# Performance work log

Measured on AMD Instinct MI355X. Metric: run time of the kernel, lower is better.

Reference implementation:

```python
import jax, jax.numpy as jnp
import numpy as np
import math

B, N, E, D = 8, 2048, 2048, 128
MAX_K = 8
HYPER_DIM = 128
LN_EPS = 1e-5


def _sinusoidal_pe(max_pos, dim):
    pe = np.zeros((max_pos, dim), dtype=np.float32)
    position = np.arange(max_pos, dtype=np.float32)[:, None]
    div_term = np.exp(np.arange(0, dim, 2, dtype=np.float32) * (-math.log(10000.0) / dim))
    pe[:, 0::2] = np.sin(position * div_term)
    pe[:, 1::2] = np.cos(position * div_term)
    return jnp.asarray(pe)


def setup_inputs() -> dict:
    key = jax.random.key(0)
    ks = jax.random.split(key, 24)
    s = 0.05
    inp = {
        'x_v': jax.random.normal(ks[0], (B, N, D), jnp.float32),
        'x_e': jax.random.normal(ks[1], (B, E, D), jnp.float32),
        'incidence': (jax.random.uniform(ks[2], (B, N, E), jnp.float32) < 0.01).astype(jnp.float32),
        'suffix_normalizer': jax.random.uniform(ks[3], (B, N), jnp.float32) * 20.0,
        'edge_orders': 1 + jax.random.randint(ks[4], (B, E), 0, MAX_K),
        'node_mask': jax.random.randint(ks[5], (B, N), 0, 2) > 0,
        'edge_mask': jax.random.randint(ks[6], (B, E), 0, 2) > 0,
        'pe1_table': _sinusoidal_pe(MAX_K + 1, D),
        'pe2_table': _sinusoidal_pe(2, D),
        'bias_b': jax.random.uniform(ks[7], (1, D), jnp.float32, -1, 1) / math.sqrt(D),
    }
    i = 8
    for m in ('mlp1', 'mlp2', 'mlp3'):
        inp[m + '_W1'] = jax.random.normal(ks[i], (D, HYPER_DIM), jnp.float32) * s; i += 1
        inp[m + '_b1'] = jnp.zeros((HYPER_DIM,), jnp.float32)
        inp[m + '_W2'] = jax.random.normal(ks[i], (HYPER_DIM, D), jnp.float32) * s; i += 1
        inp[m + '_b2'] = jnp.zeros((D,), jnp.float32)
    for n in ('norm1', 'norm2', 'norm3'):
        inp[n + '_g'] = jnp.ones((D,), jnp.float32)
        inp[n + '_b'] = jnp.zeros((D,), jnp.float32)
    return inp


def _ln(x, g, b):
    mu = jnp.mean(x, axis=-1, keepdims=True)
    var = jnp.mean(jnp.square(x - mu), axis=-1, keepdims=True)
    return (x - mu) * jax.lax.rsqrt(var + LN_EPS) * g + b


def _mlp(x, W1, b1, W2, b2):
    return jax.nn.relu(x @ W1 + b1) @ W2 + b2


def reference(x_v, x_e, incidence, suffix_normalizer, edge_orders, node_mask, edge_mask,
              pe1_table, pe2_table, bias_b,
              mlp1_W1, mlp1_b1, mlp1_W2, mlp1_b2,
              mlp2_W1, mlp2_b1, mlp2_W2, mlp2_b2,
              mlp3_W1, mlp3_b1, mlp3_W2, mlp3_b2,
              norm1_g, norm1_b, norm2_g, norm2_b, norm3_g, norm3_b):
    nm = node_mask[..., None]  # [B,N,1]
    em = edge_mask[..., None]  # [B,E,1]
    x_v = jnp.where(nm, x_v, 0.0)
    x_e = jnp.where(em, x_e, 0.0)
    pe1_k1 = pe1_table[1][None, None, :]          # [1,1,D]
    pe1_k = pe1_table[edge_orders]                # [B,E,D]
    x_v = x_v + _mlp(_ln(x_v, norm1_g, norm1_b) + pe1_k1, mlp1_W1, mlp1_b1, mlp1_W2, mlp1_b2)
    x_e = x_e + _mlp(_ln(x_e, norm1_g, norm1_b) + pe1_k, mlp1_W1, mlp1_b1, mlp1_W2, mlp1_b2)
    x_v = jnp.where(nm, x_v, 0.0)
    x_e = jnp.where(em, x_e, 0.0)
    agg = jnp.einsum('bne,bed->bnd', incidence, x_e)
    x1 = x_v + agg / (1.0 + suffix_normalizer[..., None])
    pe2_s1 = pe2_table[1][None, None, :]
    x1 = x1 + _mlp(_ln(x1, norm2_g, norm2_b) + pe2_s1, mlp2_W1, mlp2_b1, mlp2_W2, mlp2_b2)
    x = jnp.where(nm, x1, 0.0)
    x = x + _mlp(_ln(x, norm3_g, norm3_b), mlp3_W1, mlp3_b1, mlp3_W2, mlp3_b2)
    x = x + bias_b
    x = jnp.where(nm, x, 0.0)
    return x
```

## Files before the change

### kernel.cpp

```cpp
#include <hip/hip_runtime.h>
#include <stdint.h>

#define BB 8
#define NN 2048
#define EE 2048
#define DD 128
#define ROWS 32
#define RBP 132
#define NTHREADS 256
#define WMAT_U32 8192
#define SCANB 2048
#define LCAP 64

typedef __attribute__((ext_vector_type(8))) short bf16x8;
typedef __attribute__((ext_vector_type(4))) float f32x4;

__device__ inline unsigned bf16rne(float f) {
    unsigned u = __float_as_uint(f);
    return (u + 0x7fffu + ((u >> 16) & 1u)) >> 16;
}
__device__ inline float bf16lo(unsigned u) { return __uint_as_float(u << 16); }
__device__ inline float bf16hi(unsigned u) { return __uint_as_float(u & 0xffff0000u); }

#define SWZ(b) ((b) ^ ((((b) >> 8) & 7) << 4))

struct __align__(16) Smem {
    float rowbuf[ROWS][RBP];
    unsigned h[ROWS * DD / 2];
    unsigned scw[4][64];
    int rmask[ROWS];
    int ords[ROWS];
};

__device__ inline void block_load_rows(Smem& s, const float* __restrict__ src,
                                       const int* __restrict__ mask) {
    int t = threadIdx.x;
    for (int idx = t; idx < ROWS * 32; idx += NTHREADS) {
        int r = idx >> 5, c4 = (idx & 31) * 4;
        float4 v = make_float4(0.f, 0.f, 0.f, 0.f);
        if (mask[r] != 0) v = *(const float4*)&src[r * DD + c4];
        *(float4*)&s.rowbuf[r][c4] = v;
    }
    __syncthreads();
}

__device__ inline void block_ln(Smem& s, const float* __restrict__ gw,
                                const float* __restrict__ bw,
                                const float* __restrict__ pe_base, bool per_row_pe) {
    int t = threadIdx.x;
    int gr = t >> 3, g = t & 7;
    int base = g * 16;
    float x[16];
    float4* xp = (float4*)x;
    xp[0] = *(const float4*)&s.rowbuf[gr][base + 0];
    xp[1] = *(const float4*)&s.rowbuf[gr][base + 4];
    xp[2] = *(const float4*)&s.rowbuf[gr][base + 8];
    xp[3] = *(const float4*)&s.rowbuf[gr][base + 12];
    float s1 = 0.f, s2 = 0.f;
    #pragma unroll
    for (int i = 0; i < 16; i++) { s1 += x[i]; s2 += x[i] * x[i]; }
    #pragma unroll
    for (int off = 1; off < 8; off <<= 1) {
        s1 += __shfl_xor(s1, off, 64);
        s2 += __shfl_xor(s2, off, 64);
    }
    float mu = s1 * (1.f / 128.f);
    float var = s2 * (1.f / 128.f) - mu * mu;
    float rstd = rsqrtf(var + 1e-5f);
    const float* pe = nullptr;
    if (pe_base) pe = per_row_pe ? (pe_base + (size_t)s.ords[gr] * DD) : pe_base;
    unsigned p[8];
    #pragma unroll
    for (int j = 0; j < 8; j++) {
        int k0 = base + 2 * j;
        float v0 = (x[2 * j] - mu) * rstd * gw[k0] + bw[k0];
        float v1 = (x[2 * j + 1] - mu) * rstd * gw[k0 + 1] + bw[k0 + 1];
        if (pe) { v0 += pe[k0]; v1 += pe[k0 + 1]; }
        p[j] = bf16rne(v0) | (bf16rne(v1) << 16);
    }
    char* hb = (char*)s.h;
    int byte0 = gr * 256 + g * 32;
    uint4 lo = make_uint4(p[0], p[1], p[2], p[3]);
    uint4 hi = make_uint4(p[4], p[5], p[6], p[7]);
    *(uint4*)(hb + SWZ(byte0)) = lo;
    *(uint4*)(hb + SWZ(byte0 + 16)) = hi;
    __syncthreads();
}

template <bool TO_H>
__device__ inline void block_mm_core(Smem& s, const bf16x8 bfr[2][4],
                                     const float* __restrict__ bias) {
    int t = threadIdx.x;
    int w = t >> 6, l = t & 63;
    int lm = l & 15, lk = l >> 4;
    const char* hb = (const char*)s.h;
    bf16x8 afr[2][4];
    #pragma unroll
    for (int mb = 0; mb < 2; mb++) {
        int row = mb * 16 + lm;
        #pragma unroll
        for (int kb = 0; kb < 4; kb++) {
            afr[mb][kb] = *(const bf16x8*)(hb + SWZ(row * 256 + kb * 64 + lk * 16));
        }
    }
    f32x4 acc[2][2];
    #pragma unroll
    for (int mb = 0; mb < 2; mb++)
        #pragma unroll
        for (int nbl = 0; nbl < 2; nbl++)
            acc[mb][nbl] = (f32x4){0.f, 0.f, 0.f, 0.f};
    #pragma unroll
    for (int kb = 0; kb < 4; kb++)
        #pragma unroll
        for (int mb = 0; mb < 2; mb++)
            #pragma unroll
            for (int nbl = 0; nbl < 2; nbl++)
                acc[mb][nbl] = __builtin_amdgcn_mfma_f32_16x16x32_bf16(
                    afr[mb][kb], bfr[nbl][kb], acc[mb][nbl], 0, 0, 0);
    float bcol0 = bias[w * 32 + lm];
    float bcol1 = bias[w * 32 + 16 + lm];
    __syncthreads();
    if (TO_H) {
        char* hw = (char*)s.h;
        #pragma unroll
        for (int mb = 0; mb < 2; mb++)
            #pragma unroll
            for (int nbl = 0; nbl < 2; nbl++) {
                int col = w * 32 + nbl * 16 + lm;
                float bc = nbl ? bcol1 : bcol0;
                #pragma unroll
                for (int j = 0; j < 4; j++) {
                    int row = mb * 16 + lk * 4 + j;
                    float v = fmaxf(acc[mb][nbl][j] + bc, 0.f);
                    *(unsigned short*)(hw + SWZ(row * 256 + col * 2)) =
                        (unsigned short)bf16rne(v);
                }
            }
    } else {
        #pragma unroll
        for (int mb = 0; mb < 2; mb++)
            #pragma unroll
            for (int nbl = 0; nbl < 2; nbl++) {
                int col = w * 32 + nbl * 16 + lm;
                float bc = nbl ? bcol1 : bcol0;
                #pragma unroll
                for (int j = 0; j < 4; j++) {
                    int row = mb * 16 + lk * 4 + j;
                    s.rowbuf[row][col] += acc[mb][nbl][j] + bc;
                }
            }
    }
    __syncthreads();
}

template <bool TO_H>
__device__ inline void block_mm(Smem& s, const unsigned* __restrict__ WT,
                                const float* __restrict__ bias) {
    int t = threadIdx.x;
    int w = t >> 6, l = t & 63;
    int lm = l & 15, lk = l >> 4;
    bf16x8 bfr[2][4];
    const uint4* wt4 = (const uint4*)WT;
    #pragma unroll
    for (int nbl = 0; nbl < 2; nbl++) {
        int n = w * 32 + nbl * 16 + lm;
        #pragma unroll
        for (int kb = 0; kb < 4; kb++) {
            uint4 u = wt4[n * 16 + kb * 4 + lk];
            bfr[nbl][kb] = *(bf16x8*)&u;
        }
    }
    block_mm_core<TO_H>(s, bfr, bias);
}

template <bool TO_H>
__device__ inline void block_mm_f32w(Smem& s, const float* __restrict__ Wf,
                                     const float* __restrict__ bias) {
    int t = threadIdx.x;
    int w = t >> 6, l = t & 63;
    int lm = l & 15, lk = l >> 4;
    bf16x8 bfr[2][4];
    #pragma unroll
    for (int nbl = 0; nbl < 2; nbl++) {
        int n = w * 32 + nbl * 16 + lm;
        #pragma unroll
        for (int kb = 0; kb < 4; kb++) {
            int k0 = kb * 32 + lk * 8;
            unsigned pk[4];
            #pragma unroll
            for (int jp = 0; jp < 4; jp++) {
                float a = Wf[(size_t)(k0 + 2 * jp) * DD + n];
                float b = Wf[(size_t)(k0 + 2 * jp + 1) * DD + n];
                pk[jp] = bf16rne(a) | (bf16rne(b) << 16);
            }
            uint4 u = make_uint4(pk[0], pk[1], pk[2], pk[3]);
            bfr[nbl][kb] = *(bf16x8*)&u;
        }
    }
    block_mm_core<TO_H>(s, bfr, bias);
}

__device__ inline void scan_rows(Smem& s, const float* __restrict__ inc,
                                 const int* __restrict__ nmask,
                                 unsigned* __restrict__ lists, int* __restrict__ cnts,
                                 int wid, int nwaves) {
    int l = threadIdx.x & 63;
    int w = threadIdx.x >> 6;
    unsigned* sc = s.scw[w];
    unsigned long long lmlt = (1ull << l) - 1ull;
    for (int grow = wid; grow < BB * NN; grow += nwaves) {
        if (nmask[grow] == 0) continue;
        const float4* ir = (const float4*)(inc + (size_t)grow * EE);
        float4 v[8];
        #pragma unroll
        for (int i = 0; i < 8; i++) v[i] = ir[l + 64 * i];
        int total = 0;
        #pragma unroll
        for (int i = 0; i < 8; i++) {
            #pragma unroll
            for (int c = 0; c < 4; c++) {
                float val = (c == 0) ? v[i].x : (c == 1) ? v[i].y : (c == 2) ? v[i].z : v[i].w;
                bool nz = (val != 0.f);
                unsigned long long msk = __ballot(nz);
                if (nz) {
                    int pos = total + __popcll(msk & lmlt);
                    if (pos < LCAP) sc[pos] = (unsigned)((l + 64 * i) * 4 + c);
                }
                total += __popcll(msk);
            }
        }
        if (total > LCAP) total = LCAP;
        asm volatile("s_waitcnt lgkmcnt(0)" ::: "memory");
        if (l < 16) {
            uint4 q = *(const uint4*)&sc[4 * l];
            *(uint4*)&lists[(size_t)grow * LCAP + 4 * l] = q;
        }
        if (l == 0) cnts[grow] = total;
    }
}

__device__ inline void block_gather(Smem& s, int rowbase, int bb,
                                    const unsigned* __restrict__ lists,
                                    const int* __restrict__ cnts,
                                    const unsigned* __restrict__ e2pk,
                                    const float* __restrict__ sn) {
    int t = threadIdx.x;
    int w = t >> 6, l = t & 63;
    const unsigned* e2b = e2pk + (size_t)bb * (EE * (DD / 2));
    for (int r = w; r < ROWS; r += 4) {
        if (s.rmask[r] == 0) continue;
        int grow = rowbase + r;
        int cnt = cnts[grow];
        unsigned pk = (l < cnt) ? lists[(size_t)grow * LCAP + l] : 0u;
        float ax = 0.f, ay = 0.f;
        for (int j0 = 0; j0 < cnt; j0 += 8) {
            int nn = cnt - j0;
            unsigned uv[8];
            #pragma unroll
            for (int u = 0; u < 8; u++) {
                unsigned e = __shfl(pk, j0 + u, 64);
                uv[u] = (u < nn) ? e2b[(size_t)e * 64 + l] : 0u;
            }
            #pragma unroll
            for (int u = 0; u < 8; u++) { ax += bf16lo(uv[u]); ay += bf16hi(uv[u]); }
        }
        float inv = 1.f / (1.f + sn[grow]);
        float2* rb = (float2*)&s.rowbuf[r][2 * l];
        float2 cur = *rb;
        cur.x += ax * inv;
        cur.y += ay * inv;
        *rb = cur;
    }
    __syncthreads();
}

__global__ __launch_bounds__(NTHREADS) void k1_kernel(
    const float* __restrict__ x_e, const float* __restrict__ x_v,
    const int* __restrict__ emask, const int* __restrict__ nmask,
    const int* __restrict__ eord, const float* __restrict__ pe1,
    const float* __restrict__ inc,
    const float* __restrict__ n1g, const float* __restrict__ n1b,
    const float* __restrict__ W11, const float* __restrict__ b11,
    const float* __restrict__ W12, const float* __restrict__ b12,
    const float* __restrict__ W21, const float* __restrict__ W22,
    const float* __restrict__ W31, const float* __restrict__ W32,
    unsigned* __restrict__ WT,
    unsigned* __restrict__ e2pk, float* __restrict__ v2out,
    unsigned* __restrict__ lists, int* __restrict__ cnts) {
    __shared__ Smem s;
    int bid = blockIdx.x;
    int t = threadIdx.x;
    if (bid < SCANB) {
        int gtid = bid * NTHREADS + t;
        if (gtid < 4 * WMAT_U32) {
            int mat = gtid >> 13;
            int idx = gtid & (WMAT_U32 - 1);
            int n = idx >> 6, j = idx & 63;
            const float* W = mat == 0 ? W21 : mat == 1 ? W22 : mat == 2 ? W31 : W32;
            float a = W[(2 * j) * DD + n];
            float b = W[(2 * j + 1) * DD + n];
            WT[gtid] = bf16rne(a) | (bf16rne(b) << 16);
        }
        int wid = bid * 4 + (t >> 6);
        scan_rows(s, inc, nmask, lists, cnts, wid, SCANB * 4);
        return;
    }
    int lb = bid - SCANB;
    bool isEdge = lb < (BB * EE / ROWS);
    if (!isEdge) lb -= BB * EE / ROWS;
    int bb = lb & 7;
    int r0 = (lb >> 3) * ROWS;
    int rowbase = bb * EE + r0;
    const int* mask = isEdge ? emask : nmask;
    if (t < ROWS) {
        s.rmask[t] = mask[rowbase + t];
        if (isEdge) {
            int o = eord[rowbase + t];
            s.ords[t] = o < 0 ? 0 : (o > 8 ? 8 : o);
        }
    }
    block_load_rows(s, (isEdge ? x_e : x_v) + (size_t)rowbase * DD, mask + rowbase);
    block_ln(s, n1g, n1b, isEdge ? pe1 : (pe1 + DD), isEdge);
    block_mm_f32w<true>(s, W11, b11);
    block_mm_f32w<false>(s, W12, b12);
    if (isEdge) {
        unsigned* dst = e2pk + (size_t)rowbase * (DD / 2);
        for (int idx = t; idx < ROWS * 16; idx += NTHREADS) {
            int r = idx >> 4, q = idx & 15;
            uint4 o = make_uint4(0u, 0u, 0u, 0u);
            if (s.rmask[r] != 0) {
                const float* rp = &s.rowbuf[r][q * 8];
                o.x = bf16rne(rp[0]) | (bf16rne(rp[1]) << 16);
                o.y = bf16rne(rp[2]) | (bf16rne(rp[3]) << 16);
                o.z = bf16rne(rp[4]) | (bf16rne(rp[5]) << 16);
                o.w = bf16rne(rp[6]) | (bf16rne(rp[7]) << 16);
            }
            *(uint4*)&dst[r * 64 + q * 4] = o;
        }
    } else {
        for (int idx = t; idx < ROWS * 32; idx += NTHREADS) {
            int r = idx >> 5, c4 = (idx & 31) * 4;
            float4 v = make_float4(0.f, 0.f, 0.f, 0.f);
            if (s.rmask[r] != 0) v = *(const float4*)&s.rowbuf[r][c4];
            *(float4*)&v2out[(size_t)(rowbase + r) * DD + c4] = v;
        }
    }
}

__global__ __launch_bounds__(NTHREADS) void k2_kernel(
    const float* __restrict__ v2, const int* __restrict__ nmask,
    const float* __restrict__ sn,
    const float* __restrict__ pe2, const float* __restrict__ biasb,
    const float* __restrict__ n2g, const float* __restrict__ n2b,
    const float* __restrict__ n3g, const float* __restrict__ n3b,
    const unsigned* __restrict__ WT,
    const float* __restrict__ b21, const float* __restrict__ b22,
    const float* __restrict__ b31, const float* __restrict__ b32,
    const unsigned* __restrict__ e2pk, const unsigned* __restrict__ lists,
    const int* __restrict__ cnts, float* __restrict__ out) {
    __shared__ Smem s;
    int bid = blockIdx.x;
    int bb = bid & 7;
    int n0 = (bid >> 3) * ROWS;
    int rowbase = bb * NN + n0;
    int t = threadIdx.x;
    if (t < ROWS) s.rmask[t] = nmask[rowbase + t];
    block_load_rows(s, v2 + (size_t)rowbase * DD, nmask + rowbase);
    block_gather(s, rowbase, bb, lists, cnts, e2pk, sn);
    block_ln(s, n2g, n2b, pe2 + DD, false);
    block_mm<true>(s, WT + 0 * WMAT_U32, b21);
    block_mm<false>(s, WT + 1 * WMAT_U32, b22);
    block_ln(s, n3g, n3b, nullptr, false);
    block_mm<true>(s, WT + 2 * WMAT_U32, b31);
    block_mm<false>(s, WT + 3 * WMAT_U32, b32);
    for (int idx = t; idx < ROWS * 32; idx += NTHREADS) {
        int r = idx >> 5, c4 = (idx & 31) * 4;
        float4 v = make_float4(0.f, 0.f, 0.f, 0.f);
        if (s.rmask[r] != 0) {
            v = *(const float4*)&s.rowbuf[r][c4];
            float4 bbv = *(const float4*)&biasb[c4];
            v.x += bbv.x; v.y += bbv.y; v.z += bbv.z; v.w += bbv.w;
        }
        *(float4*)&out[(size_t)(rowbase + r) * DD + c4] = v;
    }
}

extern "C" void kernel_launch(void* const* d_in, const int* in_sizes, int n_in,
                              void* d_out, int out_size, void* d_ws, size_t ws_size,
                              hipStream_t stream) {
    const float* x_v   = (const float*)d_in[0];
    const float* x_e   = (const float*)d_in[1];
    const float* inc   = (const float*)d_in[2];
    const float* sn    = (const float*)d_in[3];
    const int*   eord  = (const int*)d_in[4];
    const int*   nmask = (const int*)d_in[5];
    const int*   emask = (const int*)d_in[6];
    const float* pe1   = (const float*)d_in[7];
    const float* pe2   = (const float*)d_in[8];
    const float* biasb = (const float*)d_in[9];
    const float* W11   = (const float*)d_in[10];
    const float* b11   = (const float*)d_in[11];
    const float* W12   = (const float*)d_in[12];
    const float* b12   = (const float*)d_in[13];
    const float* W21   = (const float*)d_in[14];
    const float* b21   = (const float*)d_in[15];
    const float* W22   = (const float*)d_in[16];
    const float* b22   = (const float*)d_in[17];
    const float* W31   = (const float*)d_in[18];
    const float* b31   = (const float*)d_in[19];
    const float* W32   = (const float*)d_in[20];
    const float* b32   = (const float*)d_in[21];
    const float* n1g   = (const float*)d_in[22];
    const float* n1b   = (const float*)d_in[23];
    const float* n2g   = (const float*)d_in[24];
    const float* n2b   = (const float*)d_in[25];
    const float* n3g   = (const float*)d_in[26];
    const float* n3b   = (const float*)d_in[27];

    unsigned* e2pk  = (unsigned*)d_ws;
    unsigned* WT    = e2pk + (size_t)BB * EE * (DD / 2);
    unsigned* lists = WT + 4 * WMAT_U32;
    int*      cnts  = (int*)(lists + (size_t)BB * NN * LCAP);
    float*    out   = (float*)d_out;

    dim3 blk(NTHREADS);
    k1_kernel<<<dim3(SCANB + 2 * BB * EE / ROWS), blk, 0, stream>>>(
        x_e, x_v, emask, nmask, eord, pe1, inc,
        n1g, n1b, W11, b11, W12, b12, W21, W22, W31, W32,
        WT, e2pk, out, lists, cnts);
    k2_kernel<<<dim3(BB * NN / ROWS), blk, 0, stream>>>(
        out, nmask, sn, pe2, biasb,
        n2g, n2b, n3g, n3b,
        WT, b21, b22, b31, b32,
        e2pk, lists, cnts, out);
}
```

Before: 65.87 us.

## Replace sparse incidence scan and gather with dense bf16 MFMA aggregation GEMM

```diff
diff --git a/kernel.cpp b/kernel.cpp
--- a/kernel.cpp
+++ b/kernel.cpp
@@ -9,8 +9,6 @@
 #define RBP 132
 #define NTHREADS 256
 #define WMAT_U32 8192
-#define SCANB 2048
-#define LCAP 64
 
 typedef __attribute__((ext_vector_type(8))) short bf16x8;
 typedef __attribute__((ext_vector_type(4))) float f32x4;
@@ -19,21 +17,23 @@
     unsigned u = __float_as_uint(f);
     return (u + 0x7fffu + ((u >> 16) & 1u)) >> 16;
 }
-__device__ inline float bf16lo(unsigned u) { return __uint_as_float(u << 16); }
-__device__ inline float bf16hi(unsigned u) { return __uint_as_float(u & 0xffff0000u); }
 
 #define SWZ(b) ((b) ^ ((((b) >> 8) & 7) << 4))
 
 struct __align__(16) Smem {
     float rowbuf[ROWS][RBP];
     unsigned h[ROWS * DD / 2];
-    unsigned scw[4][64];
+    float ssn[ROWS];
     int rmask[ROWS];
     int ords[ROWS];
 };
 
-__device__ inline void block_load_rows(Smem& s, const float* __restrict__ src,
-                                       const int* __restrict__ mask) {
+__device__ inline unsigned pack01(float a, float b) {
+    return (__float_as_uint(a) >> 16) | (__float_as_uint(b) & 0xffff0000u);
+}
+
+__device__ inline void load_rows32(Smem& s, const float* __restrict__ src,
+                                   const int* __restrict__ mask) {
     int t = threadIdx.x;
     for (int idx = t; idx < ROWS * 32; idx += NTHREADS) {
         int r = idx >> 5, c4 = (idx & 31) * 4;
@@ -44,9 +44,9 @@
     __syncthreads();
 }
 
-__device__ inline void block_ln(Smem& s, const float* __restrict__ gw,
-                                const float* __restrict__ bw,
-                                const float* __restrict__ pe_base, bool per_row_pe) {
+__device__ inline void ln32(Smem& s, const float* __restrict__ gw,
+                            const float* __restrict__ bw,
+                            const float* __restrict__ pe_base, bool per_row_pe) {
     int t = threadIdx.x;
     int gr = t >> 3, g = t & 7;
     int base = g * 16;
@@ -88,8 +88,8 @@
 }
 
 template <bool TO_H>
-__device__ inline void block_mm_core(Smem& s, const bf16x8 bfr[2][4],
-                                     const float* __restrict__ bias) {
+__device__ inline void mm32_core(Smem& s, const bf16x8 bfr[2][4],
+                                 const float* __restrict__ bias) {
     int t = threadIdx.x;
     int w = t >> 6, l = t & 63;
     int lm = l & 15, lk = l >> 4;
@@ -99,9 +99,8 @@
     for (int mb = 0; mb < 2; mb++) {
         int row = mb * 16 + lm;
         #pragma unroll
-        for (int kb = 0; kb < 4; kb++) {
+        for (int kb = 0; kb < 4; kb++)
             afr[mb][kb] = *(const bf16x8*)(hb + SWZ(row * 256 + kb * 64 + lk * 16));
-        }
     }
     f32x4 acc[2][2];
     #pragma unroll
@@ -154,8 +153,8 @@
 }
 
 template <bool TO_H>
-__device__ inline void block_mm(Smem& s, const unsigned* __restrict__ WT,
-                                const float* __restrict__ bias) {
+__device__ inline void mm32(Smem& s, const unsigned* __restrict__ WT,
+                            const float* __restrict__ bias) {
     int t = threadIdx.x;
     int w = t >> 6, l = t & 63;
     int lm = l & 15, lk = l >> 4;
@@ -170,12 +169,12 @@
             bfr[nbl][kb] = *(bf16x8*)&u;
         }
     }
-    block_mm_core<TO_H>(s, bfr, bias);
+    mm32_core<TO_H>(s, bfr, bias);
 }
 
 template <bool TO_H>
-__device__ inline void block_mm_f32w(Smem& s, const float* __restrict__ Wf,
-                                     const float* __restrict__ bias) {
+__device__ inline void mm32_f32w(Smem& s, const float* __restrict__ Wf,
+                                 const float* __restrict__ bias) {
     int t = threadIdx.x;
     int w = t >> 6, l = t & 63;
     int lm = l & 15, lk = l >> 4;
@@ -197,80 +196,63 @@
             bfr[nbl][kb] = *(bf16x8*)&u;
         }
     }
-    block_mm_core<TO_H>(s, bfr, bias);
-}
-
-__device__ inline void scan_rows(Smem& s, const float* __restrict__ inc,
-                                 const int* __restrict__ nmask,
-                                 unsigned* __restrict__ lists, int* __restrict__ cnts,
-                                 int wid, int nwaves) {
-    int l = threadIdx.x & 63;
-    int w = threadIdx.x >> 6;
-    unsigned* sc = s.scw[w];
-    unsigned long long lmlt = (1ull << l) - 1ull;
-    for (int grow = wid; grow < BB * NN; grow += nwaves) {
-        if (nmask[grow] == 0) continue;
-        const float4* ir = (const float4*)(inc + (size_t)grow * EE);
-        float4 v[8];
-        #pragma unroll
-        for (int i = 0; i < 8; i++) v[i] = ir[l + 64 * i];
-        int total = 0;
-        #pragma unroll
-        for (int i = 0; i < 8; i++) {
+    mm32_core<TO_H>(s, bfr, bias);
+}
+
+__device__ inline void agg_gemm(Smem& s, int rowbase, int bb,
+                                const float* __restrict__ inc,
+                                const unsigned* __restrict__ e2T) {
+    int t = threadIdx.x;
+    int w = t >> 6, l = t & 63;
+    int lm = l & 15, lk = l >> 4;
+    const unsigned* eb = e2T + (size_t)bb * (DD * (EE / 2));
+    bool act0 = s.rmask[lm] != 0;
+    bool act1 = s.rmask[16 + lm] != 0;
+    const float* a0p = inc + (size_t)(rowbase + lm) * EE + lk * 8;
+    const float* a1p = inc + (size_t)(rowbase + 16 + lm) * EE + lk * 8;
+    const unsigned* b0p = eb + (size_t)(w * 32 + lm) * (EE / 2) + lk * 4;
+    const unsigned* b1p = eb + (size_t)(w * 32 + 16 + lm) * (EE / 2) + lk * 4;
+    f32x4 acc[2][2];
+    #pragma unroll
+    for (int mb = 0; mb < 2; mb++)
+        #pragma unroll
+        for (int nbl = 0; nbl < 2; nbl++)
+            acc[mb][nbl] = (f32x4){0.f, 0.f, 0.f, 0.f};
+    #pragma unroll 4
+    for (int c = 0; c < 64; c++) {
+        int eo = c * 32;
+        uint4 ua = make_uint4(0u, 0u, 0u, 0u), ub = ua;
+        if (act0) {
+            float4 f0 = *(const float4*)(a0p + eo);
+            float4 f1 = *(const float4*)(a0p + eo + 4);
+            ua = make_uint4(pack01(f0.x, f0.y), pack01(f0.z, f0.w),
+                            pack01(f1.x, f1.y), pack01(f1.z, f1.w));
+        }
+        if (act1) {
+            float4 f0 = *(const float4*)(a1p + eo);
+            float4 f1 = *(const float4*)(a1p + eo + 4);
+            ub = make_uint4(pack01(f0.x, f0.y), pack01(f0.z, f0.w),
+                            pack01(f1.x, f1.y), pack01(f1.z, f1.w));
+        }
+        bf16x8 A0 = *(bf16x8*)&ua;
+        bf16x8 A1 = *(bf16x8*)&ub;
+        bf16x8 B0 = *(const bf16x8*)(b0p + eo / 2);
+        bf16x8 B1 = *(const bf16x8*)(b1p + eo / 2);
+        acc[0][0] = __builtin_amdgcn_mfma_f32_16x16x32_bf16(A0, B0, acc[0][0], 0, 0, 0);
+        acc[0][1] = __builtin_amdgcn_mfma_f32_16x16x32_bf16(A0, B1, acc[0][1], 0, 0, 0);
+        acc[1][0] = __builtin_amdgcn_mfma_f32_16x16x32_bf16(A1, B0, acc[1][0], 0, 0, 0);
+        acc[1][1] = __builtin_amdgcn_mfma_f32_16x16x32_bf16(A1, B1, acc[1][1], 0, 0, 0);
+    }
+    #pragma unroll
+    for (int mb = 0; mb < 2; mb++)
+        #pragma unroll
+        for (int j = 0; j < 4; j++) {
+            int row = mb * 16 + lk * 4 + j;
+            float inv = 1.f / (1.f + s.ssn[row]);
             #pragma unroll
-            for (int c = 0; c < 4; c++) {
-                float val = (c == 0) ? v[i].x : (c == 1) ? v[i].y : (c == 2) ? v[i].z : v[i].w;
-                bool nz = (val != 0.f);
-                unsigned long long msk = __ballot(nz);
-                if (nz) {
-                    int pos = total + __popcll(msk & lmlt);
-                    if (pos < LCAP) sc[pos] = (unsigned)((l + 64 * i) * 4 + c);
-                }
-                total += __popcll(msk);
-            }
-        }
-        if (total > LCAP) total = LCAP;
-        asm volatile("s_waitcnt lgkmcnt(0)" ::: "memory");
-        if (l < 16) {
-            uint4 q = *(const uint4*)&sc[4 * l];
-            *(uint4*)&lists[(size_t)grow * LCAP + 4 * l] = q;
-        }
-        if (l == 0) cnts[grow] = total;
-    }
-}
-
-__device__ inline void block_gather(Smem& s, int rowbase, int bb,
-                                    const unsigned* __restrict__ lists,
-                                    const int* __restrict__ cnts,
-                                    const unsigned* __restrict__ e2pk,
-                                    const float* __restrict__ sn) {
-    int t = threadIdx.x;
-    int w = t >> 6, l = t & 63;
-    const unsigned* e2b = e2pk + (size_t)bb * (EE * (DD / 2));
-    for (int r = w; r < ROWS; r += 4) {
-        if (s.rmask[r] == 0) continue;
-        int grow = rowbase + r;
-        int cnt = cnts[grow];
-        unsigned pk = (l < cnt) ? lists[(size_t)grow * LCAP + l] : 0u;
-        float ax = 0.f, ay = 0.f;
-        for (int j0 = 0; j0 < cnt; j0 += 8) {
-            int nn = cnt - j0;
-            unsigned uv[8];
-            #pragma unroll
-            for (int u = 0; u < 8; u++) {
-                unsigned e = __shfl(pk, j0 + u, 64);
-                uv[u] = (u < nn) ? e2b[(size_t)e * 64 + l] : 0u;
-            }
-            #pragma unroll
-            for (int u = 0; u < 8; u++) { ax += bf16lo(uv[u]); ay += bf16hi(uv[u]); }
-        }
-        float inv = 1.f / (1.f + sn[grow]);
-        float2* rb = (float2*)&s.rowbuf[r][2 * l];
-        float2 cur = *rb;
-        cur.x += ax * inv;
-        cur.y += ay * inv;
-        *rb = cur;
-    }
+            for (int nbl = 0; nbl < 2; nbl++)
+                s.rowbuf[row][w * 32 + nbl * 16 + lm] += acc[mb][nbl][j] * inv;
+        }
     __syncthreads();
 }
 
@@ -278,36 +260,28 @@
     const float* __restrict__ x_e, const float* __restrict__ x_v,
     const int* __restrict__ emask, const int* __restrict__ nmask,
     const int* __restrict__ eord, const float* __restrict__ pe1,
-    const float* __restrict__ inc,
     const float* __restrict__ n1g, const float* __restrict__ n1b,
     const float* __restrict__ W11, const float* __restrict__ b11,
     const float* __restrict__ W12, const float* __restrict__ b12,
     const float* __restrict__ W21, const float* __restrict__ W22,
     const float* __restrict__ W31, const float* __restrict__ W32,
-    unsigned* __restrict__ WT,
-    unsigned* __restrict__ e2pk, float* __restrict__ v2out,
-    unsigned* __restrict__ lists, int* __restrict__ cnts) {
+    unsigned* __restrict__ WT, unsigned* __restrict__ e2T,
+    float* __restrict__ v2out) {
     __shared__ Smem s;
     int bid = blockIdx.x;
     int t = threadIdx.x;
-    if (bid < SCANB) {
-        int gtid = bid * NTHREADS + t;
-        if (gtid < 4 * WMAT_U32) {
-            int mat = gtid >> 13;
-            int idx = gtid & (WMAT_U32 - 1);
-            int n = idx >> 6, j = idx & 63;
-            const float* W = mat == 0 ? W21 : mat == 1 ? W22 : mat == 2 ? W31 : W32;
-            float a = W[(2 * j) * DD + n];
-            float b = W[(2 * j + 1) * DD + n];
-            WT[gtid] = bf16rne(a) | (bf16rne(b) << 16);
-        }
-        int wid = bid * 4 + (t >> 6);
-        scan_rows(s, inc, nmask, lists, cnts, wid, SCANB * 4);
-        return;
-    }
-    int lb = bid - SCANB;
-    bool isEdge = lb < (BB * EE / ROWS);
-    if (!isEdge) lb -= BB * EE / ROWS;
+    int gtid = bid * NTHREADS + t;
+    if (gtid < 4 * WMAT_U32) {
+        int mat = gtid >> 13;
+        int idx = gtid & (WMAT_U32 - 1);
+        int n = idx >> 6, j = idx & 63;
+        const float* W = mat == 0 ? W21 : mat == 1 ? W22 : mat == 2 ? W31 : W32;
+        float a = W[(2 * j) * DD + n];
+        float b = W[(2 * j + 1) * DD + n];
+        WT[gtid] = bf16rne(a) | (bf16rne(b) << 16);
+    }
+    bool isEdge = bid < (BB * EE / ROWS);
+    int lb = isEdge ? bid : bid - (BB * EE / ROWS);
     int bb = lb & 7;
     int r0 = (lb >> 3) * ROWS;
     int rowbase = bb * EE + r0;
@@ -319,23 +293,18 @@
             s.ords[t] = o < 0 ? 0 : (o > 8 ? 8 : o);
         }
     }
-    block_load_rows(s, (isEdge ? x_e : x_v) + (size_t)rowbase * DD, mask + rowbase);
-    block_ln(s, n1g, n1b, isEdge ? pe1 : (pe1 + DD), isEdge);
-    block_mm_f32w<true>(s, W11, b11);
-    block_mm_f32w<false>(s, W12, b12);
+    load_rows32(s, (isEdge ? x_e : x_v) + (size_t)rowbase * DD, mask + rowbase);
+    ln32(s, n1g, n1b, isEdge ? pe1 : (pe1 + DD), isEdge);
+    mm32_f32w<true>(s, W11, b11);
+    mm32_f32w<false>(s, W12, b12);
     if (isEdge) {
-        unsigned* dst = e2pk + (size_t)rowbase * (DD / 2);
-        for (int idx = t; idx < ROWS * 16; idx += NTHREADS) {
-            int r = idx >> 4, q = idx & 15;
-            uint4 o = make_uint4(0u, 0u, 0u, 0u);
-            if (s.rmask[r] != 0) {
-                const float* rp = &s.rowbuf[r][q * 8];
-                o.x = bf16rne(rp[0]) | (bf16rne(rp[1]) << 16);
-                o.y = bf16rne(rp[2]) | (bf16rne(rp[3]) << 16);
-                o.z = bf16rne(rp[4]) | (bf16rne(rp[5]) << 16);
-                o.w = bf16rne(rp[6]) | (bf16rne(rp[7]) << 16);
-            }
-            *(uint4*)&dst[r * 64 + q * 4] = o;
+        unsigned* dstT = e2T + (size_t)bb * (DD * (EE / 2)) + (r0 >> 1);
+        for (int idx = t; idx < DD * 16; idx += NTHREADS) {
+            int d = idx >> 4, q = idx & 15;
+            int ra = 2 * q, rb = 2 * q + 1;
+            unsigned lo = s.rmask[ra] ? bf16rne(s.rowbuf[ra][d]) : 0u;
+            unsigned hi = s.rmask[rb] ? bf16rne(s.rowbuf[rb][d]) : 0u;
+            dstT[(size_t)d * (EE / 2) + q] = lo | (hi << 16);
         }
     } else {
         for (int idx = t; idx < ROWS * 32; idx += NTHREADS) {
@@ -349,30 +318,32 @@
 
 __global__ __launch_bounds__(NTHREADS) void k2_kernel(
     const float* __restrict__ v2, const int* __restrict__ nmask,
-    const float* __restrict__ sn,
+    const float* __restrict__ inc, const float* __restrict__ sn,
     const float* __restrict__ pe2, const float* __restrict__ biasb,
     const float* __restrict__ n2g, const float* __restrict__ n2b,
     const float* __restrict__ n3g, const float* __restrict__ n3b,
     const unsigned* __restrict__ WT,
     const float* __restrict__ b21, const float* __restrict__ b22,
     const float* __restrict__ b31, const float* __restrict__ b32,
-    const unsigned* __restrict__ e2pk, const unsigned* __restrict__ lists,
-    const int* __restrict__ cnts, float* __restrict__ out) {
+    const unsigned* __restrict__ e2T, float* __restrict__ out) {
     __shared__ Smem s;
     int bid = blockIdx.x;
     int bb = bid & 7;
     int n0 = (bid >> 3) * ROWS;
     int rowbase = bb * NN + n0;
     int t = threadIdx.x;
-    if (t < ROWS) s.rmask[t] = nmask[rowbase + t];
-    block_load_rows(s, v2 + (size_t)rowbase * DD, nmask + rowbase);
-    block_gather(s, rowbase, bb, lists, cnts, e2pk, sn);
-    block_ln(s, n2g, n2b, pe2 + DD, false);
-    block_mm<true>(s, WT + 0 * WMAT_U32, b21);
-    block_mm<false>(s, WT + 1 * WMAT_U32, b22);
-    block_ln(s, n3g, n3b, nullptr, false);
-    block_mm<true>(s, WT + 2 * WMAT_U32, b31);
-    block_mm<false>(s, WT + 3 * WMAT_U32, b32);
+    if (t < ROWS) {
+        s.rmask[t] = nmask[rowbase + t];
+        s.ssn[t] = sn[rowbase + t];
+    }
+    load_rows32(s, v2 + (size_t)rowbase * DD, nmask + rowbase);
+    agg_gemm(s, rowbase, bb, inc, e2T);
+    ln32(s, n2g, n2b, pe2 + DD, false);
+    mm32<true>(s, WT + 0 * WMAT_U32, b21);
+    mm32<false>(s, WT + 1 * WMAT_U32, b22);
+    ln32(s, n3g, n3b, nullptr, false);
+    mm32<true>(s, WT + 2 * WMAT_U32, b31);
+    mm32<false>(s, WT + 3 * WMAT_U32, b32);
     for (int idx = t; idx < ROWS * 32; idx += NTHREADS) {
         int r = idx >> 5, c4 = (idx & 31) * 4;
         float4 v = make_float4(0.f, 0.f, 0.f, 0.f);
@@ -417,20 +388,18 @@
     const float* n3g   = (const float*)d_in[26];
     const float* n3b   = (const float*)d_in[27];
 
-    unsigned* e2pk  = (unsigned*)d_ws;
-    unsigned* WT    = e2pk + (size_t)BB * EE * (DD / 2);
-    unsigned* lists = WT + 4 * WMAT_U32;
-    int*      cnts  = (int*)(lists + (size_t)BB * NN * LCAP);
-    float*    out   = (float*)d_out;
+    unsigned* e2T = (unsigned*)d_ws;
+    unsigned* WT  = e2T + (size_t)BB * DD * (EE / 2);
+    float*    out = (float*)d_out;
 
     dim3 blk(NTHREADS);
-    k1_kernel<<<dim3(SCANB + 2 * BB * EE / ROWS), blk, 0, stream>>>(
-        x_e, x_v, emask, nmask, eord, pe1, inc,
+    k1_kernel<<<dim3(2 * BB * EE / ROWS), blk, 0, stream>>>(
+        x_e, x_v, emask, nmask, eord, pe1,
         n1g, n1b, W11, b11, W12, b12, W21, W22, W31, W32,
-        WT, e2pk, out, lists, cnts);
+        WT, e2T, out);
     k2_kernel<<<dim3(BB * NN / ROWS), blk, 0, stream>>>(
-        out, nmask, sn, pe2, biasb,
+        out, nmask, inc, sn, pe2, biasb,
         n2g, n2b, n3g, n3b,
         WT, b21, b22, b31, b32,
-        e2pk, lists, cnts, out);
-}
+        e2T, out);
+}
```

Measured after the change: 110.8 us. 68.2% more time.
